# Kernel optimization log

Hardware: AMD Instinct MI355X
Metric: run time of the kernel (lower is better)

The kernel has to match this reference:

```python
import jax, jax.numpy as jnp
import numpy as np

P, M, B, H, D, O = 32, 32, 128, 256, 54, 53  # priorN, modernN, batch, hidden, input_dim, output_dim


def _lstm(x, Wih, Whh, b, hsz):
    """Standard torch-style LSTM (gate order i,f,g,o). x: [T,B,D] -> hs [T,B,hsz]."""
    Bn = x.shape[1]

    def step(carry, xt):
        h, c = carry
        g = xt @ Wih.T + h @ Whh.T + b
        i, f, gg, o = jnp.split(g, 4, axis=-1)
        c = jax.nn.sigmoid(f) * c + jax.nn.sigmoid(i) * jnp.tanh(gg)
        h = jax.nn.sigmoid(o) * jnp.tanh(c)
        return (h, c), h

    init = (jnp.zeros((Bn, hsz), x.dtype), jnp.zeros((Bn, hsz), x.dtype))
    _, hs = jax.lax.scan(step, init, x)
    return hs


def setup_inputs() -> dict:
    key = jax.random.key(0)
    ks = jax.random.split(key, 12)
    s = 0.1  # weight scale for numerically tame LSTMs
    src_idx = jax.random.randint(ks[0], (P, B), 0, O)
    tgt_idx = jax.random.randint(ks[1], (M, B), 0, O)
    return {
        "source_onehot": jax.nn.one_hot(src_idx, D, dtype=jnp.float32),
        "target_onehot": jax.nn.one_hot(tgt_idx, D, dtype=jnp.float32),
        "Wih_pf": jax.random.normal(ks[2], (4 * H, D), jnp.float32) * s,
        "Whh_pf": jax.random.normal(ks[3], (4 * H, H), jnp.float32) * s,
        "b_pf": jnp.zeros((4 * H,), jnp.float32),
        "Wih_pb": jax.random.normal(ks[4], (4 * H, D), jnp.float32) * s,
        "Whh_pb": jax.random.normal(ks[5], (4 * H, H), jnp.float32) * s,
        "b_pb": jnp.zeros((4 * H,), jnp.float32),
        "Wih_m": jax.random.normal(ks[6], (8 * H, D), jnp.float32) * s,
        "Whh_m": jax.random.normal(ks[7], (8 * H, 2 * H), jnp.float32) * s,
        "b_m": jnp.zeros((8 * H,), jnp.float32),
        "W_sub": jax.random.normal(ks[8], (O, 2 * H), jnp.float32) * s,
        "b_sub": jnp.zeros((O,), jnp.float32),
        "W_ins": jax.random.normal(ks[9], (O, 2 * H), jnp.float32) * s,
        "b_ins": jnp.zeros((O,), jnp.float32),
        "targets_idx": tgt_idx.astype(jnp.int32),
    }


def reference(source_onehot, target_onehot, Wih_pf, Whh_pf, b_pf, Wih_pb, Whh_pb, b_pb,
              Wih_m, Whh_m, b_m, W_sub, b_sub, W_ins, b_ins, targets_idx):
    # Bidirectional prior encoder -> [P, B, 2H]
    prior = jnp.concatenate(
        [_lstm(source_onehot, Wih_pf, Whh_pf, b_pf, H),
         _lstm(source_onehot[::-1], Wih_pb, Whh_pb, b_pb, H)[::-1]], axis=-1)
    # Unidirectional modern encoder with hidden 2H -> [M, B, 2H]
    modern = _lstm(target_onehot, Wih_m, Whh_m, b_m, 2 * H)
    # Broadcast outer-sum of contexts: [P, M, B, 2H]
    ctx = prior[:, None] + modern[None]
    sub = jax.nn.log_softmax(ctx @ W_sub.T + b_sub, axis=-1)  # [P,M,B,O]
    ins = jax.nn.log_softmax(ctx @ W_ins.T + b_ins, axis=-1)
    # log one-hots of targets (time steps 1:, vocab channels :-1): [M-1, B, O]
    logOH = jnp.where(targets_idx[1:, :, None] == jnp.arange(O)[None, None, :], 0.0, -1e30)
    p_del = sub[..., O - 1]                                     # [P,M,B]
    p_end = ins[..., O - 1]                                     # [P,M,B]
    p_sub = jax.nn.logsumexp(sub[:, :-1] + logOH[None], axis=-1)  # [P,M-1,B]
    p_ins = jax.nn.logsumexp(ins[:, :-1] + logOH[None], axis=-1)  # [P,M-1,B]
    return (p_del, p_end, p_sub, p_ins)
```

## Files before the change

kernel.cpp:

```cpp
#include <hip/hip_runtime.h>
#include <hip/hip_bf16.h>


#define PLEN 32
#define MLEN 32
#define BATCH 128
#define HP 256
#define HMOD 512
#define DIN 54
#define OUTV 53
#define NWGS 256

typedef __bf16 bf16x8 __attribute__((ext_vector_type(8)));
typedef float f32x4 __attribute__((ext_vector_type(4)));
typedef int i32x4 __attribute__((ext_vector_type(4)));

#define WS_CNT      0
#define WS_SRCIDX   1024
#define WS_WHH_PF   17408
#define WS_WHH_PB   541696
#define WS_WHH_M    1065984
#define WS_WSUB     3163136
#define WS_WINS     3228672
#define WS_HF       3294208
#define WS_HB       5391360
#define WS_HM       7488512
#define WS_SPS      11682816
#define WS_SPI      12731392
#define WS_SMS      13779968
#define WS_SMI      14828544

#define OFF_END 131072
#define OFF_SUB 262144
#define OFF_INS 389120

__device__ __forceinline__ float sigf(float x) { return 1.0f / (1.0f + __expf(-x)); }
__device__ __forceinline__ float tanhfast(float x) {
  x = fminf(15.0f, fmaxf(-15.0f, x));
  float e = __expf(2.0f * x);
  return (e - 1.0f) / (e + 1.0f);
}

__device__ __forceinline__ i32x4 load_l2_16(const void* p) {
  i32x4 r;
  asm volatile("global_load_dwordx4 %0, %1, off sc0" : "=v"(r) : "v"(p) : "memory");
  return r;
}
__device__ __forceinline__ void store_l2_short(void* p, unsigned v) {
  asm volatile("global_store_short %0, %1, off sc0" :: "v"(p), "v"(v) : "memory");
}
__device__ __forceinline__ void store_l2_dword(void* p, unsigned v) {
  asm volatile("global_store_dword %0, %1, off sc0" :: "v"(p), "v"(v) : "memory");
}
__device__ __forceinline__ unsigned load_l2_dword(const void* p) {
  unsigned v;
  asm volatile("global_load_dword %0, %1, off sc0\n\ts_waitcnt vmcnt(0)"
               : "=v"(v) : "v"(p) : "memory");
  return v;
}

#define VMWAIT(n) do { asm volatile("s_waitcnt vmcnt(" #n ")" ::: "memory"); \
                       __builtin_amdgcn_sched_barrier(0); } while (0)

__global__ void prep_kernel(const float* __restrict__ Whh_pf, const float* __restrict__ Whh_pb,
                            const float* __restrict__ Whh_m,
                            const float* __restrict__ W_sub, const float* __restrict__ W_ins,
                            const float* __restrict__ src_oh,
                            __hip_bfloat16* __restrict__ whh_pf_b, __hip_bfloat16* __restrict__ whh_pb_b,
                            __hip_bfloat16* __restrict__ whh_m_b,
                            __hip_bfloat16* __restrict__ wsub_b, __hip_bfloat16* __restrict__ wins_b,
                            int* __restrict__ src_idx)
{
  int tid = blockIdx.x * blockDim.x + threadIdx.x;
  int stride = gridDim.x * blockDim.x;
  for (int k = tid; k < 4 * HP * HP; k += stride) {
    whh_pf_b[k] = __float2bfloat16(Whh_pf[k]);
    whh_pb_b[k] = __float2bfloat16(Whh_pb[k]);
  }
  for (int k = tid; k < 4 * HMOD * HMOD; k += stride)
    whh_m_b[k] = __float2bfloat16(Whh_m[k]);
  for (int k = tid; k < 64 * HMOD; k += stride) {
    int r = k >> 9, c = k & 511;
    wsub_b[k] = __float2bfloat16(r < OUTV ? W_sub[r * HMOD + c] : 0.0f);
    wins_b[k] = __float2bfloat16(r < OUTV ? W_ins[r * HMOD + c] : 0.0f);
  }
  for (int k = tid; k < PLEN * BATCH; k += stride) {
    const float* row = src_oh + (size_t)k * DIN;
    int idx = 0;
    for (int j = 0; j < DIN; ++j) if (row[j] > 0.5f) idx = j;
    src_idx[k] = idx;
  }
}


#define DO_QUARTER(Q0)                                                          \
  _Pragma("unroll")                                                             \
  for (int kk2 = 0; kk2 < NK / 4; ++kk2) {                                      \
    bf16x8 a0 = __builtin_bit_cast(bf16x8, a[0][(Q0) + kk2]);                   \
    bf16x8 a1 = __builtin_bit_cast(bf16x8, a[1][(Q0) + kk2]);                   \
    _Pragma("unroll")                                                           \
    for (int g = 0; g < 4; ++g) {                                               \
      bf16x8 bfr = *reinterpret_cast<const bf16x8*>(                            \
          ldsB + ((((Q0) + kk2) * 4 + g) * 64 + lane) * 16);                    \
      acc[0][g] = __builtin_amdgcn_mfma_f32_16x16x32_bf16(a0, bfr, acc[0][g], 0, 0, 0); \
      acc[1][g] = __builtin_amdgcn_mfma_f32_16x16x32_bf16(a1, bfr, acc[1][g], 0, 0, 0); \
    }                                                                           \
  }

template<int H, int NWG, bool REV>
__device__ __forceinline__ void lstm_body(
    const float* __restrict__ wih, const float* __restrict__ bias,
    const int* __restrict__ idx, const __hip_bfloat16* __restrict__ whh,
    __hip_bfloat16* __restrict__ hist, unsigned* flags, int wgl, char* ldsB)
{
  constexpr int NK = H / 32;
  constexpr int CPR = H / 8;
  const int tid = threadIdx.x;
  const int lane = tid & 63;
  const int wv = tid >> 6;
  const int l15 = lane & 15;
  const int kg = lane >> 4;
  const int col = wgl * 16 + l15;
  const int bt0 = wv * 2;
  const int aoff = l15 * 32 + kg * 8;
  const int kgc  = (wgl & 1) * 2 + (l15 >> 3);
  const int jj   = l15 & 7;
  const int kkw  = wgl >> 1;

  for (int ch = tid; ch < 64 * CPR; ch += 256) {
    int r = ch / CPR, cb = ch % CPR;
    int g = r >> 4, c = r & 15;
    int kk = cb >> 2, kg2 = cb & 3;
    i32x4 v = *reinterpret_cast<const i32x4*>(
        reinterpret_cast<const char*>(whh) + ((size_t)(g * H + wgl * 16 + c) * H) * 2 + cb * 16);
    *reinterpret_cast<i32x4*>(ldsB + (((kk * 4 + g) * 64) + kg2 * 16 + c) * 16) = v;
  }

  float bgate[4];
  #pragma unroll
  for (int g = 0; g < 4; ++g) bgate[g] = bias[g * H + col];

  float cst[2][4];
  #pragma unroll
  for (int i = 0; i < 2; ++i)
    #pragma unroll
    for (int r = 0; r < 4; ++r) cst[i][r] = 0.f;

  __syncthreads();

  for (int t = 0; t < 32; ++t) {
    int tin = REV ? (31 - t) : t;

    float win[2][4][4];
    #pragma unroll
    for (int bt = 0; bt < 2; ++bt)
      #pragma unroll
      for (int r = 0; r < 4; ++r) {
        int b = (bt0 + bt) * 16 + kg * 4 + r;
        int ii = idx[tin * BATCH + b];
        #pragma unroll
        for (int g = 0; g < 4; ++g)
          win[bt][r][g] = wih[(size_t)(g * H + col) * DIN + ii] + bgate[g];
      }

    f32x4 acc[2][4];
    #pragma unroll
    for (int i = 0; i < 2; ++i)
      #pragma unroll
      for (int g = 0; g < 4; ++g) acc[i][g] = (f32x4){0.f, 0.f, 0.f, 0.f};

    if (t > 0) {
      if (wv == 0) {
        const unsigned want = (unsigned)t;
        for (;;) {
          unsigned v = load_l2_dword(flags + (lane & (NWG - 1)));
          if (__all(v >= want)) break;
          __builtin_amdgcn_s_sleep(1);
        }
      }
      __syncthreads();
      __builtin_amdgcn_sched_barrier(0);

      const __hip_bfloat16* hp = hist;
      const size_t tb = (size_t)(t - 1) * 8;
      i32x4 a[2][NK];
      #pragma unroll
      for (int kk = 0; kk < NK; ++kk) {
        a[0][kk] = load_l2_16(hp + ((tb + bt0) * NK + kk) * 512 + aoff);
        a[1][kk] = load_l2_16(hp + ((tb + bt0 + 1) * NK + kk) * 512 + aoff);
      }
      if constexpr (NK == 16) {
        VMWAIT(24); DO_QUARTER(0);
        VMWAIT(16); DO_QUARTER(4);
        VMWAIT(8);  DO_QUARTER(8);
        VMWAIT(0);  DO_QUARTER(12);
      } else {
        VMWAIT(12); DO_QUARTER(0);
        VMWAIT(8);  DO_QUARTER(2);
        VMWAIT(4);  DO_QUARTER(4);
        VMWAIT(0);  DO_QUARTER(6);
      }
    }

    #pragma unroll
    for (int bt = 0; bt < 2; ++bt) {
      #pragma unroll
      for (int r = 0; r < 4; ++r) {
        int b = (bt0 + bt) * 16 + kg * 4 + r;
        float gi = acc[bt][0][r] + win[bt][r][0];
        float gf = acc[bt][1][r] + win[bt][r][1];
        float gg = acc[bt][2][r] + win[bt][r][2];
        float go = acc[bt][3][r] + win[bt][r][3];
        float c = sigf(gf) * cst[bt][r] + sigf(gi) * tanhfast(gg);
        cst[bt][r] = c;
        __hip_bfloat16 hv = __float2bfloat16(sigf(go) * tanhfast(c));
        unsigned hbits = (unsigned)__builtin_bit_cast(unsigned short, hv);
        int btile = bt0 + bt;
        int m = kg * 4 + r;
        __hip_bfloat16* dst = hist + ((size_t)(t * 8 + btile) * NK + kkw) * 512
                              + (m * 4 + kgc) * 8 + jj;
        store_l2_short(dst, hbits);
      }
    }
    asm volatile("s_waitcnt vmcnt(0)" ::: "memory");
    __syncthreads();
    if (tid == 0)
      store_l2_dword(flags + wgl, (unsigned)(t + 1));
  }
}

__global__ __launch_bounds__(256, 1) void lstm_kernel(
    const float* __restrict__ Wih_pf, const float* __restrict__ b_pf,
    const float* __restrict__ Wih_pb, const float* __restrict__ b_pb,
    const float* __restrict__ Wih_m,  const float* __restrict__ b_m,
    const int* __restrict__ src_idx,  const int* __restrict__ tgt_idx,
    const __hip_bfloat16* __restrict__ whh_pf_b, const __hip_bfloat16* __restrict__ whh_pb_b,
    const __hip_bfloat16* __restrict__ whh_m_b,
    __hip_bfloat16* __restrict__ hf, __hip_bfloat16* __restrict__ hb,
    __hip_bfloat16* __restrict__ hm,
    unsigned* __restrict__ ctl)
{
  __shared__ __align__(16) char ldsB[65536];

  unsigned xcc;
  asm volatile("s_getreg_b32 %0, hwreg(HW_REG_XCC_ID)" : "=s"(xcc));
  xcc &= 7;
  unsigned* srank = reinterpret_cast<unsigned*>(ldsB);
  if (threadIdx.x == 0) {
    unsigned r = __hip_atomic_fetch_add(&ctl[xcc], 1u, __ATOMIC_RELAXED, __HIP_MEMORY_SCOPE_AGENT);
    asm volatile("s_waitcnt vmcnt(0)" ::: "memory");
    __hip_atomic_fetch_add(&ctl[8], 1u, __ATOMIC_RELAXED, __HIP_MEMORY_SCOPE_AGENT);
    while (__hip_atomic_load(&ctl[8], __ATOMIC_RELAXED, __HIP_MEMORY_SCOPE_AGENT) < (unsigned)NWGS)
      __builtin_amdgcn_s_sleep(8);
    srank[0] = r;
  }
  __syncthreads();
  unsigned rank = srank[0];
  __syncthreads();

  unsigned counts[8];
  #pragma unroll
  for (int x = 0; x < 8; ++x)
    counts[x] = __hip_atomic_load(&ctl[x], __ATOMIC_RELAXED, __HIP_MEMORY_SCOPE_AGENT);

  int role = -1, wgl = 0;
  {
    unsigned rem[8];
    #pragma unroll
    for (int x = 0; x < 8; ++x) rem[x] = counts[x];
    const unsigned needs[3] = {32u, 16u, 16u};
    for (int g = 0; g < 3; ++g) {
      int best = 0;
      for (int x = 1; x < 8; ++x) if (rem[x] > rem[best]) best = x;
      unsigned base = counts[best] - rem[best];
      if ((int)xcc == best && rank >= base && rank < base + needs[g]) {
        role = g; wgl = (int)(rank - base);
      }
      rem[best] -= (rem[best] >= needs[g]) ? needs[g] : rem[best];
    }
  }
  if (role < 0) return;

  if (role == 0)
    lstm_body<HMOD, 32, false>(Wih_m, b_m, tgt_idx, whh_m_b, hm, ctl + 32, wgl, ldsB);
  else if (role == 1)
    lstm_body<HP, 16, false>(Wih_pf, b_pf, src_idx, whh_pf_b, hf, ctl + 64, wgl, ldsB);
  else
    lstm_body<HP, 16, true>(Wih_pb, b_pb, src_idx, whh_pb_b, hb, ctl + 96, wgl, ldsB);
}

__global__ __launch_bounds__(256, 1) void proj_kernel(
    const __hip_bfloat16* __restrict__ hf, const __hip_bfloat16* __restrict__ hb,
    const __hip_bfloat16* __restrict__ hm,
    const __hip_bfloat16* __restrict__ wsub_b, const __hip_bfloat16* __restrict__ wins_b,
    const float* __restrict__ b_sub, const float* __restrict__ b_ins,
    float* __restrict__ SPs, float* __restrict__ SPi,
    float* __restrict__ SMs, float* __restrict__ SMi)
{
  int wg = blockIdx.x;
  bool prior = wg < 64;
  int rowbase = (wg & 63) * 64;
  const int lane = threadIdx.x & 63;
  const int wv = threadIdx.x >> 6;
  const int l15 = lane & 15;
  const int kg = lane >> 4;
  const int frag = l15 * 32 + kg * 8;
  int arow = rowbase + wv * 16 + l15;
  int tt = arow >> 7;
  int bt = ((arow & 127) >> 4);

  f32x4 acc[2][4];
  #pragma unroll
  for (int i = 0; i < 2; ++i)
    #pragma unroll
    for (int ct = 0; ct < 4; ++ct) acc[i][ct] = (f32x4){0.f, 0.f, 0.f, 0.f};

  for (int kk = 0; kk < 16; ++kk) {
    int kb = kk * 32 + kg * 8;
    bf16x8 a;
    if (prior) {
      if (kk < 8) a = *reinterpret_cast<const bf16x8*>(hf + ((size_t)(tt * 8 + bt) * 8 + kk) * 512 + frag);
      else        a = *reinterpret_cast<const bf16x8*>(hb + ((size_t)((31 - tt) * 8 + bt) * 8 + (kk - 8)) * 512 + frag);
    } else {
      a = *reinterpret_cast<const bf16x8*>(hm + ((size_t)(tt * 8 + bt) * 16 + kk) * 512 + frag);
    }
    #pragma unroll
    for (int ct = 0; ct < 4; ++ct) {
      bf16x8 bs = *reinterpret_cast<const bf16x8*>(wsub_b + (size_t)(ct * 16 + l15) * HMOD + kb);
      bf16x8 bi = *reinterpret_cast<const bf16x8*>(wins_b + (size_t)(ct * 16 + l15) * HMOD + kb);
      acc[0][ct] = __builtin_amdgcn_mfma_f32_16x16x32_bf16(a, bs, acc[0][ct], 0, 0, 0);
      acc[1][ct] = __builtin_amdgcn_mfma_f32_16x16x32_bf16(a, bi, acc[1][ct], 0, 0, 0);
    }
  }
  #pragma unroll
  for (int ct = 0; ct < 4; ++ct) {
    int colo = ct * 16 + l15;
    #pragma unroll
    for (int r = 0; r < 4; ++r) {
      int row = rowbase + wv * 16 + kg * 4 + r;
      if (prior) {
        SPs[(size_t)row * 64 + colo] = acc[0][ct][r] + (colo < OUTV ? b_sub[colo] : 0.f);
        SPi[(size_t)row * 64 + colo] = acc[1][ct][r] + (colo < OUTV ? b_ins[colo] : 0.f);
      } else {
        SMs[(size_t)row * 64 + colo] = acc[0][ct][r];
        SMi[(size_t)row * 64 + colo] = acc[1][ct][r];
      }
    }
  }
}

__global__ __launch_bounds__(256, 1) void out_kernel(
    const float* __restrict__ SPs, const float* __restrict__ SPi,
    const float* __restrict__ SMs, const float* __restrict__ SMi,
    const int* __restrict__ tgt_idx, float* __restrict__ out)
{
  int b = blockIdx.x;
  __shared__ float sps[32][66], spi[32][66], sms[32][66], smi[32][66];
  __shared__ int tg[32];
  for (int i = threadIdx.x; i < 32 * 64; i += 256) {
    int p = i >> 6, o = i & 63;
    size_t base = ((size_t)p * BATCH + b) * 64 + o;
    sps[p][o] = SPs[base]; spi[p][o] = SPi[base];
    sms[p][o] = SMs[base]; smi[p][o] = SMi[base];
  }
  if (threadIdx.x < 32) tg[threadIdx.x] = tgt_idx[threadIdx.x * BATCH + b];
  __syncthreads();

  for (int pr = threadIdx.x; pr < PLEN * MLEN; pr += 256) {
    int p = pr >> 5, m = pr & 31;
    float mxs = -1e30f, mxi = -1e30f;
    for (int o = 0; o < OUTV; ++o) {
      mxs = fmaxf(mxs, sps[p][o] + sms[m][o]);
      mxi = fmaxf(mxi, spi[p][o] + smi[m][o]);
    }
    float ss = 0.f, si = 0.f;
    for (int o = 0; o < OUTV; ++o) {
      ss += __expf(sps[p][o] + sms[m][o] - mxs);
      si += __expf(spi[p][o] + smi[m][o] - mxi);
    }
    float lses = mxs + __logf(ss);
    float lsei = mxi + __logf(si);
    size_t pm = (size_t)(p * MLEN + m) * BATCH + b;
    out[pm] = sps[p][52] + sms[m][52] - lses;
    out[OFF_END + pm] = spi[p][52] + smi[m][52] - lsei;
    if (m < 31) {
      int ttg = tg[m + 1];
      size_t pms = (size_t)(p * 31 + m) * BATCH + b;
      out[OFF_SUB + pms] = sps[p][ttg] + sms[m][ttg] - lses;
      out[OFF_INS + pms] = spi[p][ttg] + smi[m][ttg] - lsei;
    }
  }
}

extern "C" void kernel_launch(void* const* d_in, const int* in_sizes, int n_in,
                              void* d_out, int out_size, void* d_ws, size_t ws_size,
                              hipStream_t stream) {
  const float* src_oh = (const float*)d_in[0];
  const float* Wih_pf = (const float*)d_in[2];
  const float* Whh_pf = (const float*)d_in[3];
  const float* b_pf   = (const float*)d_in[4];
  const float* Wih_pb = (const float*)d_in[5];
  const float* Whh_pb = (const float*)d_in[6];
  const float* b_pb   = (const float*)d_in[7];
  const float* Wih_m  = (const float*)d_in[8];
  const float* Whh_m  = (const float*)d_in[9];
  const float* b_m    = (const float*)d_in[10];
  const float* W_sub  = (const float*)d_in[11];
  const float* b_sub  = (const float*)d_in[12];
  const float* W_ins  = (const float*)d_in[13];
  const float* b_ins  = (const float*)d_in[14];
  const int*   tgt    = (const int*)d_in[15];

  char* ws = (char*)d_ws;
  unsigned* ctl = (unsigned*)(ws + WS_CNT);
  int* src_idx = (int*)(ws + WS_SRCIDX);
  __hip_bfloat16* whh_pf_b = (__hip_bfloat16*)(ws + WS_WHH_PF);
  __hip_bfloat16* whh_pb_b = (__hip_bfloat16*)(ws + WS_WHH_PB);
  __hip_bfloat16* whh_m_b  = (__hip_bfloat16*)(ws + WS_WHH_M);
  __hip_bfloat16* wsub_b   = (__hip_bfloat16*)(ws + WS_WSUB);
  __hip_bfloat16* wins_b   = (__hip_bfloat16*)(ws + WS_WINS);
  __hip_bfloat16* hf = (__hip_bfloat16*)(ws + WS_HF);
  __hip_bfloat16* hb = (__hip_bfloat16*)(ws + WS_HB);
  __hip_bfloat16* hm = (__hip_bfloat16*)(ws + WS_HM);
  float* SPs = (float*)(ws + WS_SPS);
  float* SPi = (float*)(ws + WS_SPI);
  float* SMs = (float*)(ws + WS_SMS);
  float* SMi = (float*)(ws + WS_SMI);

  hipMemsetAsync(ctl, 0, 1024, stream);
  prep_kernel<<<256, 256, 0, stream>>>(Whh_pf, Whh_pb, Whh_m, W_sub, W_ins, src_oh,
                                       whh_pf_b, whh_pb_b, whh_m_b, wsub_b, wins_b, src_idx);
  lstm_kernel<<<NWGS, 256, 0, stream>>>(Wih_pf, b_pf, Wih_pb, b_pb, Wih_m, b_m,
                                        src_idx, tgt, whh_pf_b, whh_pb_b, whh_m_b,
                                        hf, hb, hm, ctl);
  proj_kernel<<<128, 256, 0, stream>>>(hf, hb, hm, wsub_b, wins_b, b_sub, b_ins,
                                       SPs, SPi, SMs, SMi);
  out_kernel<<<128, 256, 0, stream>>>(SPs, SPi, SMs, SMi, tgt, (float*)d_out);
}
```

Before: 292.7 us.

## Replace persistent flag-synchronised LSTM kernel with per-timestep kernel launches

The persistent LSTM kernel, with its XCC-aware role assignment and spin-wait flags between workgroups, is replaced by 32 separate launches of a per-step kernel. Kernel boundaries now provide the cross-workgroup synchronisation, and the cell state is spilled to workspace between steps. The input-weight lookup is pre-transposed with the bias folded in during prep, so each gather reads contiguous rows. In exchange, each step pays launch overhead and must reload its Whh slice into LDS, with no L2 locality placement across XCCs.

```diff
diff --git a/kernel.cpp b/kernel.cpp
--- a/kernel.cpp
+++ b/kernel.cpp
@@ -9,13 +9,11 @@
 #define HMOD 512
 #define DIN 54
 #define OUTV 53
-#define NWGS 256
 
 typedef __bf16 bf16x8 __attribute__((ext_vector_type(8)));
 typedef float f32x4 __attribute__((ext_vector_type(4)));
 typedef int i32x4 __attribute__((ext_vector_type(4)));
 
-#define WS_CNT      0
 #define WS_SRCIDX   1024
 #define WS_WHH_PF   17408
 #define WS_WHH_PB   541696
@@ -29,6 +27,10 @@
 #define WS_SPI      12731392
 #define WS_SMS      13779968
 #define WS_SMI      14828544
+#define WS_WIHT_M   WS_SPS
+#define WS_WIHT_PF  WS_SPI
+#define WS_WIHT_PB  WS_SMS
+#define WS_CST      WS_SMI
 
 #define OFF_END 131072
 #define OFF_SUB 262144
@@ -41,22 +43,10 @@
   return (e - 1.0f) / (e + 1.0f);
 }
 
-__device__ __forceinline__ i32x4 load_l2_16(const void* p) {
+__device__ __forceinline__ i32x4 load_g16(const void* p) {
   i32x4 r;
-  asm volatile("global_load_dwordx4 %0, %1, off sc0" : "=v"(r) : "v"(p) : "memory");
+  asm volatile("global_load_dwordx4 %0, %1, off" : "=v"(r) : "v"(p) : "memory");
   return r;
-}
-__device__ __forceinline__ void store_l2_short(void* p, unsigned v) {
-  asm volatile("global_store_short %0, %1, off sc0" :: "v"(p), "v"(v) : "memory");
-}
-__device__ __forceinline__ void store_l2_dword(void* p, unsigned v) {
-  asm volatile("global_store_dword %0, %1, off sc0" :: "v"(p), "v"(v) : "memory");
-}
-__device__ __forceinline__ unsigned load_l2_dword(const void* p) {
-  unsigned v;
-  asm volatile("global_load_dword %0, %1, off sc0\n\ts_waitcnt vmcnt(0)"
-               : "=v"(v) : "v"(p) : "memory");
-  return v;
 }
 
 #define VMWAIT(n) do { asm volatile("s_waitcnt vmcnt(" #n ")" ::: "memory"); \
@@ -66,9 +56,14 @@
                             const float* __restrict__ Whh_m,
                             const float* __restrict__ W_sub, const float* __restrict__ W_ins,
                             const float* __restrict__ src_oh,
+                            const float* __restrict__ Wih_pf, const float* __restrict__ b_pf,
+                            const float* __restrict__ Wih_pb, const float* __restrict__ b_pb,
+                            const float* __restrict__ Wih_m,  const float* __restrict__ b_m,
                             __hip_bfloat16* __restrict__ whh_pf_b, __hip_bfloat16* __restrict__ whh_pb_b,
                             __hip_bfloat16* __restrict__ whh_m_b,
                             __hip_bfloat16* __restrict__ wsub_b, __hip_bfloat16* __restrict__ wins_b,
+                            float* __restrict__ wihT_m, float* __restrict__ wihT_pf,
+                            float* __restrict__ wihT_pb,
                             int* __restrict__ src_idx)
 {
   int tid = blockIdx.x * blockDim.x + threadIdx.x;
@@ -83,6 +78,15 @@
     int r = k >> 9, c = k & 511;
     wsub_b[k] = __float2bfloat16(r < OUTV ? W_sub[r * HMOD + c] : 0.0f);
     wins_b[k] = __float2bfloat16(r < OUTV ? W_ins[r * HMOD + c] : 0.0f);
+  }
+  for (int j = tid; j < DIN * 4 * HMOD; j += stride) {
+    int ii = j >> 11, c = j & 2047;
+    wihT_m[j] = Wih_m[(size_t)c * DIN + ii] + b_m[c];
+  }
+  for (int j = tid; j < DIN * 4 * HP; j += stride) {
+    int ii = j >> 10, c = j & 1023;
+    wihT_pf[j] = Wih_pf[(size_t)c * DIN + ii] + b_pf[c];
+    wihT_pb[j] = Wih_pb[(size_t)c * DIN + ii] + b_pb[c];
   }
   for (int k = tid; k < PLEN * BATCH; k += stride) {
     const float* row = src_oh + (size_t)k * DIN;
@@ -107,11 +111,28 @@
     }                                                                           \
   }
 
+#define LOAD_WIN(dst, tt)                                                       \
+  do {                                                                          \
+    int tin_ = REV ? (31 - (tt)) : (tt);                                        \
+    _Pragma("unroll")                                                           \
+    for (int bt = 0; bt < 2; ++bt) {                                            \
+      _Pragma("unroll")                                                         \
+      for (int r = 0; r < 4; ++r) {                                             \
+        int b_ = (bt0 + bt) * 16 + kg * 4 + r;                                  \
+        int ii_ = idx[tin_ * BATCH + b_];                                       \
+        const float* row_ = wihT + (size_t)ii_ * (4 * H);                       \
+        _Pragma("unroll")                                                       \
+        for (int g = 0; g < 4; ++g) dst[bt][r][g] = row_[g * H + col];          \
+      }                                                                         \
+    }                                                                           \
+  } while (0)
+
 template<int H, int NWG, bool REV>
-__device__ __forceinline__ void lstm_body(
-    const float* __restrict__ wih, const float* __restrict__ bias,
-    const int* __restrict__ idx, const __hip_bfloat16* __restrict__ whh,
-    __hip_bfloat16* __restrict__ hist, unsigned* flags, int wgl, char* ldsB)
+__device__ __forceinline__ void step_body(
+    int t, const float* __restrict__ wihT, const int* __restrict__ idx,
+    const __hip_bfloat16* __restrict__ whh,
+    __hip_bfloat16* __restrict__ hist, float* __restrict__ cth,
+    int wgl, char* ldsB)
 {
   constexpr int NK = H / 32;
   constexpr int CPR = H / 8;
@@ -123,9 +144,9 @@
   const int col = wgl * 16 + l15;
   const int bt0 = wv * 2;
   const int aoff = l15 * 32 + kg * 8;
-  const int kgc  = (wgl & 1) * 2 + (l15 >> 3);
-  const int jj   = l15 & 7;
-  const int kkw  = wgl >> 1;
+  const int kgc = (wgl & 1) * 2 + (l15 >> 3);
+  const int jj = l15 & 7;
+  const int kkw = wgl >> 1;
 
   for (int ch = tid; ch < 64 * CPR; ch += 256) {
     int r = ch / CPR, cb = ch % CPR;
@@ -136,157 +157,94 @@
     *reinterpret_cast<i32x4*>(ldsB + (((kk * 4 + g) * 64) + kg2 * 16 + c) * 16) = v;
   }
 
-  float bgate[4];
-  #pragma unroll
-  for (int g = 0; g < 4; ++g) bgate[g] = bias[g * H + col];
-
   float cst[2][4];
-  #pragma unroll
-  for (int i = 0; i < 2; ++i)
-    #pragma unroll
-    for (int r = 0; r < 4; ++r) cst[i][r] = 0.f;
-
-  __syncthreads();
-
-  for (int t = 0; t < 32; ++t) {
-    int tin = REV ? (31 - t) : t;
-
-    float win[2][4][4];
-    #pragma unroll
-    for (int bt = 0; bt < 2; ++bt)
-      #pragma unroll
-      for (int r = 0; r < 4; ++r) {
-        int b = (bt0 + bt) * 16 + kg * 4 + r;
-        int ii = idx[tin * BATCH + b];
-        #pragma unroll
-        for (int g = 0; g < 4; ++g)
-          win[bt][r][g] = wih[(size_t)(g * H + col) * DIN + ii] + bgate[g];
-      }
-
-    f32x4 acc[2][4];
+  if (t > 0) {
+    f32x4 c0 = *reinterpret_cast<const f32x4*>(cth);
+    f32x4 c1 = *reinterpret_cast<const f32x4*>(cth + 4);
+    #pragma unroll
+    for (int r = 0; r < 4; ++r) { cst[0][r] = c0[r]; cst[1][r] = c1[r]; }
+  } else {
     #pragma unroll
     for (int i = 0; i < 2; ++i)
       #pragma unroll
-      for (int g = 0; g < 4; ++g) acc[i][g] = (f32x4){0.f, 0.f, 0.f, 0.f};
-
-    if (t > 0) {
-      if (wv == 0) {
-        const unsigned want = (unsigned)t;
-        for (;;) {
-          unsigned v = load_l2_dword(flags + (lane & (NWG - 1)));
-          if (__all(v >= want)) break;
-          __builtin_amdgcn_s_sleep(1);
-        }
-      }
-      __syncthreads();
-      __builtin_amdgcn_sched_barrier(0);
-
-      const __hip_bfloat16* hp = hist;
-      const size_t tb = (size_t)(t - 1) * 8;
-      i32x4 a[2][NK];
+      for (int r = 0; r < 4; ++r) cst[i][r] = 0.f;
+  }
+
+  float win[2][4][4];
+  LOAD_WIN(win, t);
+
+  __syncthreads();
+
+  f32x4 acc[2][4];
+  #pragma unroll
+  for (int bt = 0; bt < 2; ++bt)
+    #pragma unroll
+    for (int g = 0; g < 4; ++g)
       #pragma unroll
-      for (int kk = 0; kk < NK; ++kk) {
-        a[0][kk] = load_l2_16(hp + ((tb + bt0) * NK + kk) * 512 + aoff);
-        a[1][kk] = load_l2_16(hp + ((tb + bt0 + 1) * NK + kk) * 512 + aoff);
-      }
-      if constexpr (NK == 16) {
-        VMWAIT(24); DO_QUARTER(0);
-        VMWAIT(16); DO_QUARTER(4);
-        VMWAIT(8);  DO_QUARTER(8);
-        VMWAIT(0);  DO_QUARTER(12);
-      } else {
-        VMWAIT(12); DO_QUARTER(0);
-        VMWAIT(8);  DO_QUARTER(2);
-        VMWAIT(4);  DO_QUARTER(4);
-        VMWAIT(0);  DO_QUARTER(6);
-      }
-    }
-
-    #pragma unroll
-    for (int bt = 0; bt < 2; ++bt) {
-      #pragma unroll
-      for (int r = 0; r < 4; ++r) {
-        int b = (bt0 + bt) * 16 + kg * 4 + r;
-        float gi = acc[bt][0][r] + win[bt][r][0];
-        float gf = acc[bt][1][r] + win[bt][r][1];
-        float gg = acc[bt][2][r] + win[bt][r][2];
-        float go = acc[bt][3][r] + win[bt][r][3];
-        float c = sigf(gf) * cst[bt][r] + sigf(gi) * tanhfast(gg);
-        cst[bt][r] = c;
-        __hip_bfloat16 hv = __float2bfloat16(sigf(go) * tanhfast(c));
-        unsigned hbits = (unsigned)__builtin_bit_cast(unsigned short, hv);
-        int btile = bt0 + bt;
-        int m = kg * 4 + r;
-        __hip_bfloat16* dst = hist + ((size_t)(t * 8 + btile) * NK + kkw) * 512
-                              + (m * 4 + kgc) * 8 + jj;
-        store_l2_short(dst, hbits);
-      }
-    }
-    asm volatile("s_waitcnt vmcnt(0)" ::: "memory");
-    __syncthreads();
-    if (tid == 0)
-      store_l2_dword(flags + wgl, (unsigned)(t + 1));
-  }
-}
-
-__global__ __launch_bounds__(256, 1) void lstm_kernel(
-    const float* __restrict__ Wih_pf, const float* __restrict__ b_pf,
-    const float* __restrict__ Wih_pb, const float* __restrict__ b_pb,
-    const float* __restrict__ Wih_m,  const float* __restrict__ b_m,
+      for (int r = 0; r < 4; ++r) acc[bt][g][r] = win[bt][r][g];
+
+  if (t > 0) {
+    const __hip_bfloat16* hp = hist;
+    const size_t tb = (size_t)(t - 1) * 8;
+    i32x4 a[2][NK];
+    #pragma unroll
+    for (int kk = 0; kk < NK; ++kk) {
+      a[0][kk] = load_g16(hp + ((tb + bt0) * NK + kk) * 512 + aoff);
+      a[1][kk] = load_g16(hp + ((tb + bt0 + 1) * NK + kk) * 512 + aoff);
+    }
+    if constexpr (NK == 16) {
+      VMWAIT(24); DO_QUARTER(0);
+      VMWAIT(16); DO_QUARTER(4);
+      VMWAIT(8);  DO_QUARTER(8);
+      VMWAIT(0);  DO_QUARTER(12);
+    } else {
+      VMWAIT(12); DO_QUARTER(0);
+      VMWAIT(8);  DO_QUARTER(2);
+      VMWAIT(4);  DO_QUARTER(4);
+      VMWAIT(0);  DO_QUARTER(6);
+    }
+  }
+
+  #pragma unroll
+  for (int bt = 0; bt < 2; ++bt) {
+    __hip_bfloat16* htile = hist + ((size_t)(t * 8 + bt0 + bt) * NK + kkw) * 512;
+    #pragma unroll
+    for (int r = 0; r < 4; ++r) {
+      float gi = acc[bt][0][r], gf = acc[bt][1][r];
+      float gg = acc[bt][2][r], go = acc[bt][3][r];
+      float c = sigf(gf) * cst[bt][r] + sigf(gi) * tanhfast(gg);
+      cst[bt][r] = c;
+      int m = kg * 4 + r;
+      htile[(m * 4 + kgc) * 8 + jj] = __float2bfloat16(sigf(go) * tanhfast(c));
+    }
+  }
+  f32x4 c0, c1;
+  #pragma unroll
+  for (int r = 0; r < 4; ++r) { c0[r] = cst[0][r]; c1[r] = cst[1][r]; }
+  *reinterpret_cast<f32x4*>(cth) = c0;
+  *reinterpret_cast<f32x4*>(cth + 4) = c1;
+}
+
+__global__ __launch_bounds__(256, 1) void lstm_step(
+    int t,
+    const float* __restrict__ wihT_m, const float* __restrict__ wihT_pf,
+    const float* __restrict__ wihT_pb,
     const int* __restrict__ src_idx,  const int* __restrict__ tgt_idx,
     const __hip_bfloat16* __restrict__ whh_pf_b, const __hip_bfloat16* __restrict__ whh_pb_b,
     const __hip_bfloat16* __restrict__ whh_m_b,
     __hip_bfloat16* __restrict__ hf, __hip_bfloat16* __restrict__ hb,
     __hip_bfloat16* __restrict__ hm,
-    unsigned* __restrict__ ctl)
+    float* __restrict__ cstate)
 {
   __shared__ __align__(16) char ldsB[65536];
-
-  unsigned xcc;
-  asm volatile("s_getreg_b32 %0, hwreg(HW_REG_XCC_ID)" : "=s"(xcc));
-  xcc &= 7;
-  unsigned* srank = reinterpret_cast<unsigned*>(ldsB);
-  if (threadIdx.x == 0) {
-    unsigned r = __hip_atomic_fetch_add(&ctl[xcc], 1u, __ATOMIC_RELAXED, __HIP_MEMORY_SCOPE_AGENT);
-    asm volatile("s_waitcnt vmcnt(0)" ::: "memory");
-    __hip_atomic_fetch_add(&ctl[8], 1u, __ATOMIC_RELAXED, __HIP_MEMORY_SCOPE_AGENT);
-    while (__hip_atomic_load(&ctl[8], __ATOMIC_RELAXED, __HIP_MEMORY_SCOPE_AGENT) < (unsigned)NWGS)
-      __builtin_amdgcn_s_sleep(8);
-    srank[0] = r;
-  }
-  __syncthreads();
-  unsigned rank = srank[0];
-  __syncthreads();
-
-  unsigned counts[8];
-  #pragma unroll
-  for (int x = 0; x < 8; ++x)
-    counts[x] = __hip_atomic_load(&ctl[x], __ATOMIC_RELAXED, __HIP_MEMORY_SCOPE_AGENT);
-
-  int role = -1, wgl = 0;
-  {
-    unsigned rem[8];
-    #pragma unroll
-    for (int x = 0; x < 8; ++x) rem[x] = counts[x];
-    const unsigned needs[3] = {32u, 16u, 16u};
-    for (int g = 0; g < 3; ++g) {
-      int best = 0;
-      for (int x = 1; x < 8; ++x) if (rem[x] > rem[best]) best = x;
-      unsigned base = counts[best] - rem[best];
-      if ((int)xcc == best && rank >= base && rank < base + needs[g]) {
-        role = g; wgl = (int)(rank - base);
-      }
-      rem[best] -= (rem[best] >= needs[g]) ? needs[g] : rem[best];
-    }
-  }
-  if (role < 0) return;
-
-  if (role == 0)
-    lstm_body<HMOD, 32, false>(Wih_m, b_m, tgt_idx, whh_m_b, hm, ctl + 32, wgl, ldsB);
-  else if (role == 1)
-    lstm_body<HP, 16, false>(Wih_pf, b_pf, src_idx, whh_pf_b, hf, ctl + 64, wgl, ldsB);
+  int wg = blockIdx.x;
+  float* cth = cstate + ((size_t)wg * 256 + threadIdx.x) * 8;
+  if (wg < 32)
+    step_body<HMOD, 32, false>(t, wihT_m, tgt_idx, whh_m_b, hm, cth, wg, ldsB);
+  else if (wg < 48)
+    step_body<HP, 16, false>(t, wihT_pf, src_idx, whh_pf_b, hf, cth, wg - 32, ldsB);
   else
-    lstm_body<HP, 16, true>(Wih_pb, b_pb, src_idx, whh_pb_b, hb, ctl + 96, wgl, ldsB);
+    step_body<HP, 16, true>(t, wihT_pb, src_idx, whh_pb_b, hb, cth, wg - 48, ldsB);
 }
 
 __global__ __launch_bounds__(256, 1) void proj_kernel(
@@ -412,7 +370,6 @@
   const int*   tgt    = (const int*)d_in[15];
 
   char* ws = (char*)d_ws;
-  unsigned* ctl = (unsigned*)(ws + WS_CNT);
   int* src_idx = (int*)(ws + WS_SRCIDX);
   __hip_bfloat16* whh_pf_b = (__hip_bfloat16*)(ws + WS_WHH_PF);
   __hip_bfloat16* whh_pb_b = (__hip_bfloat16*)(ws + WS_WHH_PB);
@@ -422,17 +379,23 @@
   __hip_bfloat16* hf = (__hip_bfloat16*)(ws + WS_HF);
   __hip_bfloat16* hb = (__hip_bfloat16*)(ws + WS_HB);
   __hip_bfloat16* hm = (__hip_bfloat16*)(ws + WS_HM);
+  float* wihT_m  = (float*)(ws + WS_WIHT_M);
+  float* wihT_pf = (float*)(ws + WS_WIHT_PF);
+  float* wihT_pb = (float*)(ws + WS_WIHT_PB);
+  float* cstate  = (float*)(ws + WS_CST);
   float* SPs = (float*)(ws + WS_SPS);
   float* SPi = (float*)(ws + WS_SPI);
   float* SMs = (float*)(ws + WS_SMS);
   float* SMi = (float*)(ws + WS_SMI);
 
-  hipMemsetAsync(ctl, 0, 1024, stream);
   prep_kernel<<<256, 256, 0, stream>>>(Whh_pf, Whh_pb, Whh_m, W_sub, W_ins, src_oh,
-                                       whh_pf_b, whh_pb_b, whh_m_b, wsub_b, wins_b, src_idx);
-  lstm_kernel<<<NWGS, 256, 0, stream>>>(Wih_pf, b_pf, Wih_pb, b_pb, Wih_m, b_m,
-                                        src_idx, tgt, whh_pf_b, whh_pb_b, whh_m_b,
-                                        hf, hb, hm, ctl);
+                                       Wih_pf, b_pf, Wih_pb, b_pb, Wih_m, b_m,
+                                       whh_pf_b, whh_pb_b, whh_m_b, wsub_b, wins_b,
+                                       wihT_m, wihT_pf, wihT_pb, src_idx);
+  for (int t = 0; t < 32; ++t)
+    lstm_step<<<64, 256, 0, stream>>>(t, wihT_m, wihT_pf, wihT_pb, src_idx, tgt,
+                                      whh_pf_b, whh_pb_b, whh_m_b,
+                                      hf, hb, hm, cstate);
   proj_kernel<<<128, 256, 0, stream>>>(hf, hb, hm, wsub_b, wins_b, b_sub, b_ins,
                                        SPs, SPi, SMs, SMi);
   out_kernel<<<128, 256, 0, stream>>>(SPs, SPi, SMs, SMi, tgt, (float*)d_out);
```

After: 356.9 us. 21.9% more time.
